# Performance work log

Measured on AMD Instinct MI355X. Metric: run time of the kernel, lower is better.

Reference implementation:

```python
import jax, jax.numpy as jnp
import numpy as np
import math

B, SQ, SKV, D = 16, 1024, 1024, 256


def setup_inputs() -> dict:
    key = jax.random.key(0)
    kq, kk, kv, km = jax.random.split(key, 4)
    # Scale inputs down: the module applies exp() to raw QK^T logits, so dot
    # products must stay small to avoid overflow (std ~ 0.05^2*sqrt(D) ~ 0.04).
    scale = 0.05
    query = jax.random.normal(kq, (B, SQ, D), dtype=jnp.float32) * scale
    key_t = jax.random.normal(kk, (B, SKV, D), dtype=jnp.float32) * scale
    value = jax.random.normal(kv, (B, SKV, D), dtype=jnp.float32)
    mask = jax.random.randint(km, (B, SQ, SKV), 0, 2, dtype=jnp.int32)
    return {"query": query, "key": key_t, "value": value, "mask": mask}


def reference(query, key, value, mask):
    # scores = exp(Q K^T) / sqrt(d)  -- note: exp BEFORE scaling, as in source
    d = query.shape[-1]
    inv_sqrt_d = jnp.float32(1.0 / math.sqrt(d))
    scores = jnp.exp(jnp.einsum('bqd,bkd->bqk', query, key)) * inv_sqrt_d
    # masked_fill(mask == 0, -1e9)
    scores = jnp.where(mask == 0, jnp.float32(-1e9), scores)
    p_attn = jax.nn.softmax(scores, axis=-1)
    # dropout is identity in eval mode (deterministic reference)
    output = jnp.einsum('bqk,bkd->bqd', p_attn, value)
    # flatten=True path: sum over the query/sequence dim
    return output.sum(axis=1), p_attn
```

## Files before the change

### kernel.cpp

```cpp
#include <hip/hip_runtime.h>

#define NB   16
#define NSQ  1024
#define NSKV 1024
#define ND   256

typedef float     f32x4  __attribute__((ext_vector_type(4)));
typedef _Float16  f16x4  __attribute__((ext_vector_type(4)));
typedef int       i32x4  __attribute__((ext_vector_type(4)));
typedef long      lng2   __attribute__((ext_vector_type(2)));

#define EST 268

template<bool HI>
__device__ __forceinline__ int pk_fp8(float a, float b, int old) {
    return __builtin_amdgcn_cvt_pk_fp8_f32(a, b, old, HI);
}

__global__ __launch_bounds__(256) void prep_kernel(
    const float* __restrict__ K, unsigned char* __restrict__ Kb8,
    const int* __restrict__ mask, unsigned* __restrict__ mw,
    float* __restrict__ colsum, float* __restrict__ out0)
{
    const int bid = blockIdx.x;
    const int tid = threadIdx.x;
    if (bid < 2048) {
        const int i    = bid * 256 + tid;
        const int lane = i & 63;
        const int m    = lane & 15;
        const int kg   = lane >> 4;
        const int dc   = (i >> 6) & 7;
        const int kvb  = (i >> 9) & 63;
        const int b    = i >> 15;
        const float* s = K + ((size_t)(b * NSKV + kvb * 16 + m)) * ND + dc * 32 + kg * 8;
        float4 a = *(const float4*)s;
        float4 c = *(const float4*)(s + 4);
        int lo = pk_fp8<false>(a.x, a.y, 0);
        lo     = pk_fp8<true >(a.z, a.w, lo);
        int hi = pk_fp8<false>(c.x, c.y, 0);
        hi     = pk_fp8<true >(c.z, c.w, hi);
        int2 w; w.x = lo; w.y = hi;
        const size_t obyte = ((size_t)((b * 64 + kvb) * 4 + (dc >> 1))) * 1024
                           + lane * 16 + (dc & 1) * 8;
        *(int2*)(Kb8 + obyte) = w;
    } else if (bid < 2048 + 4096) {
        const int row = (bid - 2048) * 4 + (tid >> 6);
        const int l   = tid & 63;
        const int4* mrow = (const int4*)(mask + (size_t)row * NSKV) + l * 4;
        unsigned w = 0;
        #pragma unroll
        for (int v = 0; v < 4; ++v) {
            int4 mv = mrow[v];
            w |= (mv.x != 0 ? 1u : 0u) << (v * 4 + 0);
            w |= (mv.y != 0 ? 1u : 0u) << (v * 4 + 1);
            w |= (mv.z != 0 ? 1u : 0u) << (v * 4 + 2);
            w |= (mv.w != 0 ? 1u : 0u) << (v * 4 + 3);
        }
        const int m    = l & 15;
        const int base = l & 48;
        unsigned out = 0;
        #pragma unroll
        for (int c = 0; c < 16; ++c) {
            unsigned v = (unsigned)__shfl((int)w, base | c);
            out |= ((v >> m) & 1u) << c;
        }
        mw[(size_t)row * 64 + l] = out;
    } else if (bid < 2048 + 4096 + 64) {
        colsum[(bid - 6144) * 256 + tid] = 0.f;
    } else {
        out0[(bid - 6208) * 256 + tid] = 0.f;
    }
}

__global__ __launch_bounds__(256, 4) void attn_fused(
    const float* __restrict__ Q, const unsigned char* __restrict__ Kb8,
    const unsigned* __restrict__ mw, float* __restrict__ out_p,
    float* __restrict__ colsum)
{
    const int g    = blockIdx.x;
    const int tile = ((g & 7) << 7) | (g >> 3);
    const int b    = tile >> 6;
    const int q0   = (tile & 63) * 16;
    const int tid  = threadIdx.x;
    const int lane = tid & 63;
    const int h    = tid >> 6;
    const int m    = lane & 15;
    const int kg   = lane >> 4;

    __shared__ __attribute__((aligned(16))) _Float16 epark[4][16 * EST];
    __shared__ float Zs[4][16];
    __shared__ float invZs[16];

    _Float16* myE = &epark[h][0];

    long afrag[8];
    {
        const float* qbase = Q + ((size_t)(b * NSQ + q0 + m)) * ND;
        #pragma unroll
        for (int dc = 0; dc < 8; ++dc) {
            const float* p4 = qbase + dc * 32 + kg * 8;
            float4 x = *(const float4*)(p4);
            float4 y = *(const float4*)(p4 + 4);
            int lo = pk_fp8<false>(x.x, x.y, 0);
            lo     = pk_fp8<true >(x.z, x.w, lo);
            int hi = pk_fp8<false>(y.x, y.y, 0);
            hi     = pk_fp8<true >(y.z, y.w, hi);
            afrag[dc] = (long)(((unsigned long long)(unsigned)hi << 32) | (unsigned)lo);
        }
    }

    unsigned mword[4];
    #pragma unroll
    for (int i = 0; i < 4; ++i)
        mword[i] = mw[(size_t)(b * NSQ + q0 + kg * 4 + i) * 64 + h * 16 + m];

    const char* kbase = (const char*)Kb8
                      + (size_t)(b * 64 + h * 16) * 4096 + lane * 16;

    float zacc[4] = {0.f, 0.f, 0.f, 0.f};
    i32x4 fA[4], fB[4];

    #define LD4(gr, c) { \
        const char* _p0 = kbase + (size_t)(c) * 4096; \
        asm volatile( \
            "global_load_dwordx4 %0, %4, off\n\t" \
            "global_load_dwordx4 %1, %4, off offset:1024\n\t" \
            "global_load_dwordx4 %2, %4, off offset:2048\n\t" \
            "global_load_dwordx4 %3, %4, off offset:3072" \
            : "=&v"((gr)[0]), "=&v"((gr)[1]), "=&v"((gr)[2]), "=&v"((gr)[3]) \
            : "v"(_p0) \
            : "memory"); }

    #define W4(gr) { \
        asm volatile("s_waitcnt vmcnt(4)" \
            : "+v"((gr)[0]), "+v"((gr)[1]), "+v"((gr)[2]), "+v"((gr)[3]) \
            :: "memory"); \
        __builtin_amdgcn_sched_barrier(0); }

    #define W0(gr) { \
        asm volatile("s_waitcnt vmcnt(0)" \
            : "+v"((gr)[0]), "+v"((gr)[1]), "+v"((gr)[2]), "+v"((gr)[3]) \
            :: "memory"); \
        __builtin_amdgcn_sched_barrier(0); }

    #define COMPUTE(gr, c) { \
        f32x4 acc = {0.f, 0.f, 0.f, 0.f}; \
        _Pragma("unroll") \
        for (int j = 0; j < 4; ++j) { \
            lng2 p_ = __builtin_bit_cast(lng2, (gr)[j]); \
            acc = __builtin_amdgcn_mfma_f32_16x16x32_fp8_fp8(afrag[2*j],   p_[0], acc, 0, 0, 0); \
            acc = __builtin_amdgcn_mfma_f32_16x16x32_fp8_fp8(afrag[2*j+1], p_[1], acc, 0, 0, 0); \
        } \
        _Pragma("unroll") \
        for (int i = 0; i < 4; ++i) { \
            float e = ((mword[i] >> (c)) & 1u) ? __expf(__expf(acc[i]) * 0.0625f) : 0.f; \
            zacc[i] += e; \
            myE[(kg * 4 + i) * EST + (c) * 16 + m] = (_Float16)e; \
        } }

    LD4(fA, 0);
    LD4(fB, 1);

    #pragma unroll
    for (int cc = 0; cc < 16; cc += 2) {
        W4(fA);
        COMPUTE(fA, cc);
        if (cc + 2 < 16) LD4(fA, cc + 2);
        if (cc + 2 < 16) { W4(fB); } else { W0(fB); }
        COMPUTE(fB, cc + 1);
        if (cc + 3 < 16) LD4(fB, cc + 3);
    }
    #undef LD4
    #undef W4
    #undef W0
    #undef COMPUTE

    #pragma unroll
    for (int i = 0; i < 4; ++i) {
        float z = zacc[i];
        z += __shfl_xor(z, 1);
        z += __shfl_xor(z, 2);
        z += __shfl_xor(z, 4);
        z += __shfl_xor(z, 8);
        if (m == 0) Zs[h][kg * 4 + i] = z;
    }
    __syncthreads();
    if (tid < 16)
        invZs[tid] = 1.0f / (Zs[0][tid] + Zs[1][tid] + Zs[2][tid] + Zs[3][tid]);
    __syncthreads();

    float csum[4] = {0.f, 0.f, 0.f, 0.f};
    float* prow = out_p + (size_t)(b * NSQ + q0) * NSKV + h * 256 + lane * 4;
    #pragma unroll
    for (int s = 0; s < 16; ++s) {
        f16x4 ev = *(const f16x4*)&myE[s * EST + lane * 4];
        const float iz = invZs[s];
        float4 pv;
        pv.x = (float)ev[0] * iz; pv.y = (float)ev[1] * iz;
        pv.z = (float)ev[2] * iz; pv.w = (float)ev[3] * iz;
        *(float4*)(prow + (size_t)s * NSKV) = pv;
        csum[0] += pv.x; csum[1] += pv.y; csum[2] += pv.z; csum[3] += pv.w;
    }
    #pragma unroll
    for (int j = 0; j < 4; ++j)
        atomicAdd(&colsum[b * NSKV + h * 256 + lane * 4 + j], csum[j]);
}

__global__ __launch_bounds__(256) void attn_out_kernel(
    const float* __restrict__ colsum, const float* __restrict__ V,
    float* __restrict__ out)
{
    const int b  = blockIdx.x >> 6;
    const int ks = (blockIdx.x & 63) << 4;
    const int d  = threadIdx.x;
    float acc = 0.f;
    #pragma unroll
    for (int k = 0; k < 16; ++k) {
        acc += colsum[b * NSKV + ks + k] * V[((size_t)(b * NSKV + ks + k)) * ND + d];
    }
    atomicAdd(&out[b * ND + d], acc);
}

extern "C" void kernel_launch(void* const* d_in, const int* in_sizes, int n_in,
                              void* d_out, int out_size, void* d_ws, size_t ws_size,
                              hipStream_t stream)
{
    (void)in_sizes; (void)n_in; (void)out_size; (void)ws_size;
    const float* Q    = (const float*)d_in[0];
    const float* K    = (const float*)d_in[1];
    const float* V    = (const float*)d_in[2];
    const int*   mask = (const int*)d_in[3];

    float* out0 = (float*)d_out;
    float* p    = out0 + NB * ND;

    float*         colsum = (float*)d_ws;
    unsigned char* Kb8    = (unsigned char*)d_ws + (64 << 10);
    unsigned*      mwbits = (unsigned*)((char*)d_ws + (64 << 10) + (size_t)NB * NSKV * ND);

    prep_kernel<<<6224, 256, 0, stream>>>(K, Kb8, mask, mwbits, colsum, out0);
    attn_fused<<<NB * 64, 256, 0, stream>>>(Q, Kb8, mwbits, p, colsum);
    attn_out_kernel<<<NB * 64, 256, 0, stream>>>(colsum, V, out0);
}
```

Measured before the change: 194.6 us.

## Process two 16-row query tiles per block to reuse K fragments

New measurement: 186.6 us. 1.04x faster.

```diff
diff --git a/kernel.cpp b/kernel.cpp
--- a/kernel.cpp
+++ b/kernel.cpp
@@ -72,30 +72,32 @@
     }
 }
 
-__global__ __launch_bounds__(256, 4) void attn_fused(
+__global__ __launch_bounds__(256, 2) void attn_fused(
     const float* __restrict__ Q, const unsigned char* __restrict__ Kb8,
     const unsigned* __restrict__ mw, float* __restrict__ out_p,
     float* __restrict__ colsum)
 {
     const int g    = blockIdx.x;
-    const int tile = ((g & 7) << 7) | (g >> 3);
-    const int b    = tile >> 6;
-    const int q0   = (tile & 63) * 16;
+    const int tile = ((g & 7) << 6) | (g >> 3);
+    const int b    = tile >> 5;
+    const int q0   = (tile & 31) * 32;
     const int tid  = threadIdx.x;
     const int lane = tid & 63;
     const int h    = tid >> 6;
     const int m    = lane & 15;
     const int kg   = lane >> 4;
 
-    __shared__ __attribute__((aligned(16))) _Float16 epark[4][16 * EST];
-    __shared__ float Zs[4][16];
-    __shared__ float invZs[16];
-
-    _Float16* myE = &epark[h][0];
-
-    long afrag[8];
-    {
-        const float* qbase = Q + ((size_t)(b * NSQ + q0 + m)) * ND;
+    __shared__ __attribute__((aligned(16))) _Float16 epark[2][4][16 * EST];
+    __shared__ float Zs[2][4][16];
+    __shared__ float invZs[2][16];
+
+    _Float16* myE0 = &epark[0][h][0];
+    _Float16* myE1 = &epark[1][h][0];
+
+    long afragA[8], afragB[8];
+    #pragma unroll
+    for (int sub = 0; sub < 2; ++sub) {
+        const float* qbase = Q + ((size_t)(b * NSQ + q0 + sub * 16 + m)) * ND;
         #pragma unroll
         for (int dc = 0; dc < 8; ++dc) {
             const float* p4 = qbase + dc * 32 + kg * 8;
@@ -105,19 +107,23 @@
             lo     = pk_fp8<true >(x.z, x.w, lo);
             int hi = pk_fp8<false>(y.x, y.y, 0);
             hi     = pk_fp8<true >(y.z, y.w, hi);
-            afrag[dc] = (long)(((unsigned long long)(unsigned)hi << 32) | (unsigned)lo);
-        }
-    }
-
-    unsigned mword[4];
-    #pragma unroll
-    for (int i = 0; i < 4; ++i)
-        mword[i] = mw[(size_t)(b * NSQ + q0 + kg * 4 + i) * 64 + h * 16 + m];
+            long v = (long)(((unsigned long long)(unsigned)hi << 32) | (unsigned)lo);
+            if (sub == 0) afragA[dc] = v; else afragB[dc] = v;
+        }
+    }
+
+    unsigned mwordA[4], mwordB[4];
+    #pragma unroll
+    for (int i = 0; i < 4; ++i) {
+        mwordA[i] = mw[(size_t)(b * NSQ + q0 +      kg * 4 + i) * 64 + h * 16 + m];
+        mwordB[i] = mw[(size_t)(b * NSQ + q0 + 16 + kg * 4 + i) * 64 + h * 16 + m];
+    }
 
     const char* kbase = (const char*)Kb8
                       + (size_t)(b * 64 + h * 16) * 4096 + lane * 16;
 
-    float zacc[4] = {0.f, 0.f, 0.f, 0.f};
+    float zaccA[4] = {0.f, 0.f, 0.f, 0.f};
+    float zaccB[4] = {0.f, 0.f, 0.f, 0.f};
     i32x4 fA[4], fB[4];
 
     #define LD4(gr, c) { \
@@ -144,18 +150,24 @@
         __builtin_amdgcn_sched_barrier(0); }
 
     #define COMPUTE(gr, c) { \
-        f32x4 acc = {0.f, 0.f, 0.f, 0.f}; \
+        f32x4 accA = {0.f, 0.f, 0.f, 0.f}; \
+        f32x4 accB = {0.f, 0.f, 0.f, 0.f}; \
         _Pragma("unroll") \
         for (int j = 0; j < 4; ++j) { \
             lng2 p_ = __builtin_bit_cast(lng2, (gr)[j]); \
-            acc = __builtin_amdgcn_mfma_f32_16x16x32_fp8_fp8(afrag[2*j],   p_[0], acc, 0, 0, 0); \
-            acc = __builtin_amdgcn_mfma_f32_16x16x32_fp8_fp8(afrag[2*j+1], p_[1], acc, 0, 0, 0); \
+            accA = __builtin_amdgcn_mfma_f32_16x16x32_fp8_fp8(afragA[2*j],   p_[0], accA, 0, 0, 0); \
+            accB = __builtin_amdgcn_mfma_f32_16x16x32_fp8_fp8(afragB[2*j],   p_[0], accB, 0, 0, 0); \
+            accA = __builtin_amdgcn_mfma_f32_16x16x32_fp8_fp8(afragA[2*j+1], p_[1], accA, 0, 0, 0); \
+            accB = __builtin_amdgcn_mfma_f32_16x16x32_fp8_fp8(afragB[2*j+1], p_[1], accB, 0, 0, 0); \
         } \
         _Pragma("unroll") \
         for (int i = 0; i < 4; ++i) { \
-            float e = ((mword[i] >> (c)) & 1u) ? __expf(__expf(acc[i]) * 0.0625f) : 0.f; \
-            zacc[i] += e; \
-            myE[(kg * 4 + i) * EST + (c) * 16 + m] = (_Float16)e; \
+            float eA = ((mwordA[i] >> (c)) & 1u) ? __expf(__expf(accA[i]) * 0.0625f) : 0.f; \
+            float eB = ((mwordB[i] >> (c)) & 1u) ? __expf(__expf(accB[i]) * 0.0625f) : 0.f; \
+            zaccA[i] += eA; \
+            zaccB[i] += eB; \
+            myE0[(kg * 4 + i) * EST + (c) * 16 + m] = (_Float16)eA; \
+            myE1[(kg * 4 + i) * EST + (c) * 16 + m] = (_Float16)eB; \
         } }
 
     LD4(fA, 0);
@@ -177,28 +189,49 @@
 
     #pragma unroll
     for (int i = 0; i < 4; ++i) {
-        float z = zacc[i];
-        z += __shfl_xor(z, 1);
-        z += __shfl_xor(z, 2);
-        z += __shfl_xor(z, 4);
-        z += __shfl_xor(z, 8);
-        if (m == 0) Zs[h][kg * 4 + i] = z;
+        float zA = zaccA[i];
+        zA += __shfl_xor(zA, 1);
+        zA += __shfl_xor(zA, 2);
+        zA += __shfl_xor(zA, 4);
+        zA += __shfl_xor(zA, 8);
+        float zB = zaccB[i];
+        zB += __shfl_xor(zB, 1);
+        zB += __shfl_xor(zB, 2);
+        zB += __shfl_xor(zB, 4);
+        zB += __shfl_xor(zB, 8);
+        if (m == 0) {
+            Zs[0][h][kg * 4 + i] = zA;
+            Zs[1][h][kg * 4 + i] = zB;
+        }
     }
     __syncthreads();
     if (tid < 16)
-        invZs[tid] = 1.0f / (Zs[0][tid] + Zs[1][tid] + Zs[2][tid] + Zs[3][tid]);
+        invZs[0][tid] = 1.0f / (Zs[0][0][tid] + Zs[0][1][tid] + Zs[0][2][tid] + Zs[0][3][tid]);
+    else if (tid < 32)
+        invZs[1][tid - 16] = 1.0f / (Zs[1][0][tid - 16] + Zs[1][1][tid - 16] + Zs[1][2][tid - 16] + Zs[1][3][tid - 16]);
     __syncthreads();
 
     float csum[4] = {0.f, 0.f, 0.f, 0.f};
-    float* prow = out_p + (size_t)(b * NSQ + q0) * NSKV + h * 256 + lane * 4;
+    float* prowA = out_p + (size_t)(b * NSQ + q0) * NSKV + h * 256 + lane * 4;
     #pragma unroll
     for (int s = 0; s < 16; ++s) {
-        f16x4 ev = *(const f16x4*)&myE[s * EST + lane * 4];
-        const float iz = invZs[s];
+        f16x4 ev = *(const f16x4*)&myE0[s * EST + lane * 4];
+        const float iz = invZs[0][s];
         float4 pv;
         pv.x = (float)ev[0] * iz; pv.y = (float)ev[1] * iz;
         pv.z = (float)ev[2] * iz; pv.w = (float)ev[3] * iz;
-        *(float4*)(prow + (size_t)s * NSKV) = pv;
+        *(float4*)(prowA + (size_t)s * NSKV) = pv;
+        csum[0] += pv.x; csum[1] += pv.y; csum[2] += pv.z; csum[3] += pv.w;
+    }
+    float* prowB = prowA + (size_t)16 * NSKV;
+    #pragma unroll
+    for (int s = 0; s < 16; ++s) {
+        f16x4 ev = *(const f16x4*)&myE1[s * EST + lane * 4];
+        const float iz = invZs[1][s];
+        float4 pv;
+        pv.x = (float)ev[0] * iz; pv.y = (float)ev[1] * iz;
+        pv.z = (float)ev[2] * iz; pv.w = (float)ev[3] * iz;
+        *(float4*)(prowB + (size_t)s * NSKV) = pv;
         csum[0] += pv.x; csum[1] += pv.y; csum[2] += pv.z; csum[3] += pv.w;
     }
     #pragma unroll
@@ -239,6 +272,6 @@
     unsigned*      mwbits = (unsigned*)((char*)d_ws + (64 << 10) + (size_t)NB * NSKV * ND);
 
     prep_kernel<<<6224, 256, 0, stream>>>(K, Kb8, mask, mwbits, colsum, out0);
-    attn_fused<<<NB * 64, 256, 0, stream>>>(Q, Kb8, mwbits, p, colsum);
+    attn_fused<<<512, 256, 0, stream>>>(Q, Kb8, mwbits, p, colsum);
     attn_out_kernel<<<NB * 64, 256, 0, stream>>>(colsum, V, out0);
 }
```

## Deepen K prefetch to four buffers and replace colsum atomics with partials

Applied to the files above, without the earlier changes.

Measured after the change: 185.4 us. 1.05x faster.

```diff
diff --git a/kernel.cpp b/kernel.cpp
--- a/kernel.cpp
+++ b/kernel.cpp
@@ -20,7 +20,7 @@
 __global__ __launch_bounds__(256) void prep_kernel(
     const float* __restrict__ K, unsigned char* __restrict__ Kb8,
     const int* __restrict__ mask, unsigned* __restrict__ mw,
-    float* __restrict__ colsum, float* __restrict__ out0)
+    float* __restrict__ out0)
 {
     const int bid = blockIdx.x;
     const int tid = threadIdx.x;
@@ -65,22 +65,21 @@
             out |= ((v >> m) & 1u) << c;
         }
         mw[(size_t)row * 64 + l] = out;
-    } else if (bid < 2048 + 4096 + 64) {
-        colsum[(bid - 6144) * 256 + tid] = 0.f;
     } else {
-        out0[(bid - 6208) * 256 + tid] = 0.f;
+        out0[(bid - 6144) * 256 + tid] = 0.f;
     }
 }
 
 __global__ __launch_bounds__(256, 4) void attn_fused(
     const float* __restrict__ Q, const unsigned char* __restrict__ Kb8,
     const unsigned* __restrict__ mw, float* __restrict__ out_p,
-    float* __restrict__ colsum)
+    float* __restrict__ cs_part)
 {
     const int g    = blockIdx.x;
     const int tile = ((g & 7) << 7) | (g >> 3);
     const int b    = tile >> 6;
-    const int q0   = (tile & 63) * 16;
+    const int qt   = tile & 63;
+    const int q0   = qt * 16;
     const int tid  = threadIdx.x;
     const int lane = tid & 63;
     const int h    = tid >> 6;
@@ -118,7 +117,7 @@
                       + (size_t)(b * 64 + h * 16) * 4096 + lane * 16;
 
     float zacc[4] = {0.f, 0.f, 0.f, 0.f};
-    i32x4 fA[4], fB[4];
+    i32x4 fA[4], fB[4], fC[4], fD[4];
 
     #define LD4(gr, c) { \
         const char* _p0 = kbase + (size_t)(c) * 4096; \
@@ -131,49 +130,60 @@
             : "v"(_p0) \
             : "memory"); }
 
-    #define W4(gr) { \
-        asm volatile("s_waitcnt vmcnt(4)" \
-            : "+v"((gr)[0]), "+v"((gr)[1]), "+v"((gr)[2]), "+v"((gr)[3]) \
+    #define W8P(g1, g2) { \
+        asm volatile("s_waitcnt vmcnt(8)" \
+            : "+v"((g1)[0]), "+v"((g1)[1]), "+v"((g1)[2]), "+v"((g1)[3]), \
+              "+v"((g2)[0]), "+v"((g2)[1]), "+v"((g2)[2]), "+v"((g2)[3]) \
             :: "memory"); \
         __builtin_amdgcn_sched_barrier(0); }
 
-    #define W0(gr) { \
+    #define W0P(g1, g2) { \
         asm volatile("s_waitcnt vmcnt(0)" \
-            : "+v"((gr)[0]), "+v"((gr)[1]), "+v"((gr)[2]), "+v"((gr)[3]) \
+            : "+v"((g1)[0]), "+v"((g1)[1]), "+v"((g1)[2]), "+v"((g1)[3]), \
+              "+v"((g2)[0]), "+v"((g2)[1]), "+v"((g2)[2]), "+v"((g2)[3]) \
             :: "memory"); \
         __builtin_amdgcn_sched_barrier(0); }
 
-    #define COMPUTE(gr, c) { \
-        f32x4 acc = {0.f, 0.f, 0.f, 0.f}; \
+    #define COMPUTE2(gE, gO, cE, cO) { \
+        f32x4 accE = {0.f, 0.f, 0.f, 0.f}; \
+        f32x4 accO = {0.f, 0.f, 0.f, 0.f}; \
         _Pragma("unroll") \
         for (int j = 0; j < 4; ++j) { \
-            lng2 p_ = __builtin_bit_cast(lng2, (gr)[j]); \
-            acc = __builtin_amdgcn_mfma_f32_16x16x32_fp8_fp8(afrag[2*j],   p_[0], acc, 0, 0, 0); \
-            acc = __builtin_amdgcn_mfma_f32_16x16x32_fp8_fp8(afrag[2*j+1], p_[1], acc, 0, 0, 0); \
+            lng2 pE = __builtin_bit_cast(lng2, (gE)[j]); \
+            lng2 pO = __builtin_bit_cast(lng2, (gO)[j]); \
+            accE = __builtin_amdgcn_mfma_f32_16x16x32_fp8_fp8(afrag[2*j],   pE[0], accE, 0, 0, 0); \
+            accO = __builtin_amdgcn_mfma_f32_16x16x32_fp8_fp8(afrag[2*j],   pO[0], accO, 0, 0, 0); \
+            accE = __builtin_amdgcn_mfma_f32_16x16x32_fp8_fp8(afrag[2*j+1], pE[1], accE, 0, 0, 0); \
+            accO = __builtin_amdgcn_mfma_f32_16x16x32_fp8_fp8(afrag[2*j+1], pO[1], accO, 0, 0, 0); \
         } \
         _Pragma("unroll") \
         for (int i = 0; i < 4; ++i) { \
-            float e = ((mword[i] >> (c)) & 1u) ? __expf(__expf(acc[i]) * 0.0625f) : 0.f; \
-            zacc[i] += e; \
-            myE[(kg * 4 + i) * EST + (c) * 16 + m] = (_Float16)e; \
+            float eE = ((mword[i] >> (cE)) & 1u) ? __expf(__expf(accE[i]) * 0.0625f) : 0.f; \
+            float eO = ((mword[i] >> (cO)) & 1u) ? __expf(__expf(accO[i]) * 0.0625f) : 0.f; \
+            zacc[i] += eE; \
+            zacc[i] += eO; \
+            myE[(kg * 4 + i) * EST + (cE) * 16 + m] = (_Float16)eE; \
+            myE[(kg * 4 + i) * EST + (cO) * 16 + m] = (_Float16)eO; \
         } }
 
     LD4(fA, 0);
     LD4(fB, 1);
-
-    #pragma unroll
-    for (int cc = 0; cc < 16; cc += 2) {
-        W4(fA);
-        COMPUTE(fA, cc);
-        if (cc + 2 < 16) LD4(fA, cc + 2);
-        if (cc + 2 < 16) { W4(fB); } else { W0(fB); }
-        COMPUTE(fB, cc + 1);
-        if (cc + 3 < 16) LD4(fB, cc + 3);
+    LD4(fC, 2);
+    LD4(fD, 3);
+
+    #pragma unroll
+    for (int cc = 0; cc < 16; cc += 4) {
+        W8P(fA, fB);
+        COMPUTE2(fA, fB, cc, cc + 1);
+        if (cc + 4 < 16) { LD4(fA, cc + 4); LD4(fB, cc + 5); }
+        if (cc + 4 < 16) { W8P(fC, fD); } else { W0P(fC, fD); }
+        COMPUTE2(fC, fD, cc + 2, cc + 3);
+        if (cc + 4 < 16) { LD4(fC, cc + 6); LD4(fD, cc + 7); }
     }
     #undef LD4
-    #undef W4
-    #undef W0
-    #undef COMPUTE
+    #undef W8P
+    #undef W0P
+    #undef COMPUTE2
 
     #pragma unroll
     for (int i = 0; i < 4; ++i) {
@@ -202,21 +212,39 @@
         csum[0] += pv.x; csum[1] += pv.y; csum[2] += pv.z; csum[3] += pv.w;
     }
     #pragma unroll
-    for (int j = 0; j < 4; ++j)
-        atomicAdd(&colsum[b * NSKV + h * 256 + lane * 4 + j], csum[j]);
+    for (int j = 0; j < 4; ++j) {
+        const int k = h * 256 + lane * 4 + j;
+        cs_part[((size_t)(b * NSKV + k)) * 64 + qt] = csum[j];
+    }
 }
 
 __global__ __launch_bounds__(256) void attn_out_kernel(
-    const float* __restrict__ colsum, const float* __restrict__ V,
+    const float* __restrict__ cs_part, const float* __restrict__ V,
     float* __restrict__ out)
 {
     const int b  = blockIdx.x >> 6;
     const int ks = (blockIdx.x & 63) << 4;
-    const int d  = threadIdx.x;
+    const int tid = threadIdx.x;
+
+    __shared__ float cs16[16];
+
+    {
+        const float* base = cs_part + ((size_t)(b * NSKV + ks)) * 64;
+        float4 v = *(const float4*)(base + tid * 4);
+        float s = v.x + v.y + v.z + v.w;
+        s += __shfl_xor(s, 1);
+        s += __shfl_xor(s, 2);
+        s += __shfl_xor(s, 4);
+        s += __shfl_xor(s, 8);
+        if ((tid & 15) == 0) cs16[tid >> 4] = s;
+    }
+    __syncthreads();
+
+    const int d = tid;
     float acc = 0.f;
     #pragma unroll
     for (int k = 0; k < 16; ++k) {
-        acc += colsum[b * NSKV + ks + k] * V[((size_t)(b * NSKV + ks + k)) * ND + d];
+        acc += cs16[k] * V[((size_t)(b * NSKV + ks + k)) * ND + d];
     }
     atomicAdd(&out[b * ND + d], acc);
 }
@@ -234,11 +262,11 @@
     float* out0 = (float*)d_out;
     float* p    = out0 + NB * ND;
 
-    float*         colsum = (float*)d_ws;
-    unsigned char* Kb8    = (unsigned char*)d_ws + (64 << 10);
-    unsigned*      mwbits = (unsigned*)((char*)d_ws + (64 << 10) + (size_t)NB * NSKV * ND);
-
-    prep_kernel<<<6224, 256, 0, stream>>>(K, Kb8, mask, mwbits, colsum, out0);
-    attn_fused<<<NB * 64, 256, 0, stream>>>(Q, Kb8, mwbits, p, colsum);
-    attn_out_kernel<<<NB * 64, 256, 0, stream>>>(colsum, V, out0);
-}
+    float*         cs_part = (float*)d_ws;
+    unsigned char* Kb8     = (unsigned char*)d_ws + ((size_t)NB * NSKV * 64 * 4);
+    unsigned*      mwbits  = (unsigned*)((char*)Kb8 + (size_t)NB * NSKV * ND);
+
+    prep_kernel<<<6160, 256, 0, stream>>>(K, Kb8, mask, mwbits, out0);
+    attn_fused<<<NB * 64, 256, 0, stream>>>(Q, Kb8, mwbits, p, cs_part);
+    attn_out_kernel<<<NB * 64, 256, 0, stream>>>(cs_part, V, out0);
+}
```
